# Performance work log

Measured on AMD Instinct MI355X. Metric: run time of the kernel, lower is better.

## Reference

```python
import jax, jax.numpy as jnp
import numpy as np

N, C, H, W = 8, 19, 512, 512


def setup_inputs() -> dict:
    key = jax.random.key(0)
    k1, k2 = jax.random.split(key)
    logits = jax.random.normal(k1, (N, C, H, W), dtype=jnp.float32)
    labels = jax.random.randint(k2, (N, H, W), 0, C, dtype=jnp.int32)
    return {"logits": logits, "labels": labels}


def reference(logits, labels):
    # softmax over class dim, then flatten to [P, C] (P = N*H*W)
    num_classes = logits.shape[1]
    probas = jax.nn.softmax(logits, axis=1)
    probas = jnp.moveaxis(probas, 1, -1).reshape(-1, num_classes)  # [P, C]
    labels_flat = labels.reshape(-1)  # [P]

    # fg[p, c] = 1 if labels[p] == c (ground truth, detached)
    fg = jax.nn.one_hot(labels_flat, num_classes, dtype=probas.dtype)  # [P, C]

    errors = jnp.abs(fg - probas)  # [P, C]
    # per-class descending sort of errors (vectorized over all classes)
    perm = jnp.argsort(-errors, axis=0)  # [P, C]
    errors_sorted = jnp.take_along_axis(errors, perm, axis=0)
    fg_sorted = jnp.take_along_axis(fg, perm, axis=0)

    # Lovasz gradient (Alg. 1), per class column
    gts = jnp.sum(fg_sorted, axis=0)  # [C]
    intersection = gts - jnp.cumsum(fg_sorted, axis=0)  # [P, C]
    union = gts + jnp.cumsum(1.0 - fg_sorted, axis=0)  # [P, C]
    jaccard = 1.0 - intersection / union
    grad = jnp.concatenate([jaccard[:1], jaccard[1:] - jaccard[:-1]], axis=0)

    losses = jnp.sum(errors_sorted * grad, axis=0)  # [C]
    return jnp.mean(losses)
```

## Files before the change

kernel.cpp:

```cpp
#include <hip/hip_runtime.h>

#define CLS   19
#define NBINS 128
#define HWSZ  (512 * 512)
#define NPIX  (8 * HWSZ)
#define HIST  (CLS * NBINS)
#define CSTR  (HIST + 16)
#define NC    2
#define TPB   256
#define NBLK  1024
#define GPB   ((NPIX / 4) / NBLK)

typedef float vf4 __attribute__((ext_vector_type(4)));
typedef int   vi4 __attribute__((ext_vector_type(4)));

__global__ __launch_bounds__(TPB)
void lovasz_zero(unsigned long long* __restrict__ gh, float* __restrict__ out) {
    const int t = threadIdx.x;
    for (int i = t; i < HIST; i += TPB) gh[i] = 0ull;
    if (t == 0) out[0] = 0.f;
}

__global__ __launch_bounds__(TPB)
void lovasz_hist(const float* __restrict__ logits, const int* __restrict__ labels,
                 unsigned long long* __restrict__ gh) {
    __shared__ unsigned h[NC * CSTR];
    const int tid = threadIdx.x;
    for (int i = tid; i < NC * CSTR; i += TPB) h[i] = 0u;
    __syncthreads();

    const unsigned copy = (unsigned)tid & (NC - 1);
    const int base_g = blockIdx.x * GPB;
    for (int it = 0; it < GPB; it += TPB) {
        const int g  = base_g + it + tid;
        const int p  = g << 2;
        const int n  = p >> 18;
        const int hw = p & (HWSZ - 1);
        const vf4* bp = (const vf4*)(logits + (size_t)n * CLS * HWSZ + hw);

        vf4 va[CLS];
#pragma unroll
        for (int c = 0; c < CLS; ++c)
            va[c] = __builtin_nontemporal_load(&bp[c * (HWSZ / 4)]);

        vf4 s = {0.f, 0.f, 0.f, 0.f};
#pragma unroll
        for (int c = 0; c < CLS; ++c) {
            va[c].x = __expf(va[c].x); s.x += va[c].x;
            va[c].y = __expf(va[c].y); s.y += va[c].y;
            va[c].z = __expf(va[c].z); s.z += va[c].z;
            va[c].w = __expf(va[c].w); s.w += va[c].w;
        }
        const vf4 inv = {1.f / s.x, 1.f / s.y, 1.f / s.z, 1.f / s.w};
        const vi4 lab = __builtin_nontemporal_load((const vi4*)(labels + p));

        unsigned* hc = &h[copy * CSTR];
#pragma unroll
        for (int c = 0; c < CLS; ++c) {
            float e; unsigned ic; int b;
            e = va[c].x * inv.x; ic = 1u;
            if (c == lab.x) { e = 1.f - e; ic = 0x10001u; }
            b = (int)(e * (float)NBINS); b = b > (NBINS - 1) ? (NBINS - 1) : b;
            atomicAdd(&hc[c * NBINS + b], ic);
            e = va[c].y * inv.y; ic = 1u;
            if (c == lab.y) { e = 1.f - e; ic = 0x10001u; }
            b = (int)(e * (float)NBINS); b = b > (NBINS - 1) ? (NBINS - 1) : b;
            atomicAdd(&hc[c * NBINS + b], ic);
            e = va[c].z * inv.z; ic = 1u;
            if (c == lab.z) { e = 1.f - e; ic = 0x10001u; }
            b = (int)(e * (float)NBINS); b = b > (NBINS - 1) ? (NBINS - 1) : b;
            atomicAdd(&hc[c * NBINS + b], ic);
            e = va[c].w * inv.w; ic = 1u;
            if (c == lab.w) { e = 1.f - e; ic = 0x10001u; }
            b = (int)(e * (float)NBINS); b = b > (NBINS - 1) ? (NBINS - 1) : b;
            atomicAdd(&hc[c * NBINS + b], ic);
        }
    }
    __syncthreads();
    for (int i = tid; i < HIST; i += TPB) {
        const unsigned v = h[i] + h[CSTR + i];
        if (v) {
            const unsigned long long pk =
                (unsigned long long)(v & 0xFFFFu) | ((unsigned long long)(v >> 16) << 32);
            atomicAdd(&gh[i], pk);
        }
    }
}

__global__ __launch_bounds__(NBINS)
void lovasz_final(const unsigned long long* __restrict__ gh, float* __restrict__ out) {
    __shared__ unsigned scnt[NBINS], sfg[NBINS];
    __shared__ float part[2];
    const int c = blockIdx.x, t = threadIdx.x;

    const unsigned long long v = gh[c * NBINS + t];
    scnt[t] = (unsigned)(v & 0xFFFFFFFFull);
    sfg[t]  = (unsigned)(v >> 32);
    __syncthreads();

    unsigned nb = 0, fb = 0, g = 0;
    for (int b = t + 1; b < NBINS; ++b) { nb += scnt[b]; fb += sfg[b]; }
    for (int b = 0; b < NBINS; ++b) g += sfg[b];

    const float gts = (float)g;
    const float nB = (float)nb,            fB = (float)fb;
    const float nA = nB + (float)scnt[t],  fA = fB + (float)sfg[t];
    const float dB = gts + nB - fB;
    const float jB = dB > 0.f ? 1.f - (gts - fB) / dB : 0.f;
    const float dA = gts + nA - fA;
    const float jA = dA > 0.f ? 1.f - (gts - fA) / dA : 0.f;
    float contrib = (((float)t + 0.5f) * (1.f / NBINS)) * (jA - jB);

    for (int off = 32; off > 0; off >>= 1) contrib += __shfl_down(contrib, off);
    if ((t & 63) == 0) part[t >> 6] = contrib;
    __syncthreads();
    if (t == 0) atomicAdd(out, (part[0] + part[1]) * (1.f / (float)CLS));
}

extern "C" void kernel_launch(void* const* d_in, const int* in_sizes, int n_in,
                              void* d_out, int out_size, void* d_ws, size_t ws_size,
                              hipStream_t stream) {
    const float* logits = (const float*)d_in[0];
    const int*   labels = (const int*)d_in[1];
    float*       out    = (float*)d_out;
    unsigned long long* gh = (unsigned long long*)d_ws;

    lovasz_zero<<<1, TPB, 0, stream>>>(gh, out);
    lovasz_hist<<<NBLK, TPB, 0, stream>>>(logits, labels, gh);
    lovasz_final<<<CLS, NBINS, 0, stream>>>(gh, out);
}
```

Baseline: 234.5 us.

## Fuse final Lovasz reduction into histogram kernel via last-block pattern

Removes the separate final kernel launch: each histogram block increments a global arrival counter, and the last block to arrive computes the per-class Lovasz contributions and writes the output. It also raises the number of shared-memory histogram copies from two to four to reduce atomic contention. The last-block tail runs the 19-class scan serially in one block, and the larger LDS footprint may lower occupancy.

```diff
diff --git a/kernel.cpp b/kernel.cpp
--- a/kernel.cpp
+++ b/kernel.cpp
@@ -5,8 +5,8 @@
 #define HWSZ  (512 * 512)
 #define NPIX  (8 * HWSZ)
 #define HIST  (CLS * NBINS)
-#define CSTR  (HIST + 16)
-#define NC    2
+#define CSTR  (HIST + 8)
+#define NC    4
 #define TPB   256
 #define NBLK  1024
 #define GPB   ((NPIX / 4) / NBLK)
@@ -17,14 +17,16 @@
 __global__ __launch_bounds__(TPB)
 void lovasz_zero(unsigned long long* __restrict__ gh, float* __restrict__ out) {
     const int t = threadIdx.x;
-    for (int i = t; i < HIST; i += TPB) gh[i] = 0ull;
+    for (int i = t; i <= HIST; i += TPB) gh[i] = 0ull;
     if (t == 0) out[0] = 0.f;
 }
 
 __global__ __launch_bounds__(TPB)
 void lovasz_hist(const float* __restrict__ logits, const int* __restrict__ labels,
-                 unsigned long long* __restrict__ gh) {
+                 unsigned long long* __restrict__ gh, float* __restrict__ out) {
     __shared__ unsigned h[NC * CSTR];
+    __shared__ float    part[4];
+    __shared__ unsigned s_arr;
     const int tid = threadIdx.x;
     for (int i = tid; i < NC * CSTR; i += TPB) h[i] = 0u;
     __syncthreads();
@@ -77,44 +79,64 @@
         }
     }
     __syncthreads();
+
     for (int i = tid; i < HIST; i += TPB) {
-        const unsigned v = h[i] + h[CSTR + i];
+        const unsigned v = h[i] + h[CSTR + i] + h[2 * CSTR + i] + h[3 * CSTR + i];
         if (v) {
             const unsigned long long pk =
                 (unsigned long long)(v & 0xFFFFu) | ((unsigned long long)(v >> 16) << 32);
             atomicAdd(&gh[i], pk);
         }
     }
-}
 
-__global__ __launch_bounds__(NBINS)
-void lovasz_final(const unsigned long long* __restrict__ gh, float* __restrict__ out) {
-    __shared__ unsigned scnt[NBINS], sfg[NBINS];
-    __shared__ float part[2];
-    const int c = blockIdx.x, t = threadIdx.x;
+    __threadfence();
+    __syncthreads();
+    if (tid == 0) s_arr = (unsigned)atomicAdd(&gh[HIST], 1ull);
+    __syncthreads();
+    if (s_arr != NBLK - 1) return;
 
-    const unsigned long long v = gh[c * NBINS + t];
-    scnt[t] = (unsigned)(v & 0xFFFFFFFFull);
-    sfg[t]  = (unsigned)(v >> 32);
-    __syncthreads();
+    __threadfence();
+    unsigned* scnt = h;
+    unsigned* sfg  = h + 2 * NBINS;
+    const int bin  = tid & (NBINS - 1);
+    const int half = tid >> 7;
+    float acc = 0.f;
+    for (int cb = 0; cb < CLS; cb += 2) {
+        const int c = cb + half;
+        if (c < CLS) {
+            const unsigned long long v = gh[c * NBINS + bin];
+            scnt[half * NBINS + bin] = (unsigned)(v & 0xFFFFFFFFull);
+            sfg [half * NBINS + bin] = (unsigned)(v >> 32);
+        }
+        __syncthreads();
+        if (c < CLS) {
+            unsigned nb = 0, fb = 0, g = 0;
+            for (int b = bin + 1; b < NBINS; ++b) {
+                nb += scnt[half * NBINS + b]; fb += sfg[half * NBINS + b];
+            }
+            for (int b = 0; b < NBINS; ++b) g += sfg[half * NBINS + b];
 
-    unsigned nb = 0, fb = 0, g = 0;
-    for (int b = t + 1; b < NBINS; ++b) { nb += scnt[b]; fb += sfg[b]; }
-    for (int b = 0; b < NBINS; ++b) g += sfg[b];
+            const float gts = (float)g;
+            const float nB = (float)nb,                           fB = (float)fb;
+            const float nA = nB + (float)scnt[half * NBINS + bin],
+                        fA = fB + (float)sfg [half * NBINS + bin];
+            const float dB = gts + nB - fB;
+            const float jB = dB > 0.f ? 1.f - (gts - fB) / dB : 0.f;
+            const float dA = gts + nA - fA;
+            const float jA = dA > 0.f ? 1.f - (gts - fA) / dA : 0.f;
+            float contrib = (((float)bin + 0.5f) * (1.f / NBINS)) * (jA - jB);
 
-    const float gts = (float)g;
-    const float nB = (float)nb,            fB = (float)fb;
-    const float nA = nB + (float)scnt[t],  fA = fB + (float)sfg[t];
-    const float dB = gts + nB - fB;
-    const float jB = dB > 0.f ? 1.f - (gts - fB) / dB : 0.f;
-    const float dA = gts + nA - fA;
-    const float jA = dA > 0.f ? 1.f - (gts - fA) / dA : 0.f;
-    float contrib = (((float)t + 0.5f) * (1.f / NBINS)) * (jA - jB);
-
-    for (int off = 32; off > 0; off >>= 1) contrib += __shfl_down(contrib, off);
-    if ((t & 63) == 0) part[t >> 6] = contrib;
-    __syncthreads();
-    if (t == 0) atomicAdd(out, (part[0] + part[1]) * (1.f / (float)CLS));
+            for (int off = 32; off > 0; off >>= 1) contrib += __shfl_down(contrib, off);
+            if ((tid & 63) == 0) part[tid >> 6] = contrib;
+        }
+        __syncthreads();
+        if (tid == 0) {
+            acc += (part[0] + part[1]) * (1.f / (float)CLS);
+            if (cb + 1 < CLS) acc += (part[2] + part[3]) * (1.f / (float)CLS);
+        }
+        __syncthreads();
+    }
+    if (tid == 0) out[0] = acc;
 }
 
 extern "C" void kernel_launch(void* const* d_in, const int* in_sizes, int n_in,
@@ -126,6 +148,5 @@
     unsigned long long* gh = (unsigned long long*)d_ws;
 
     lovasz_zero<<<1, TPB, 0, stream>>>(gh, out);
-    lovasz_hist<<<NBLK, TPB, 0, stream>>>(logits, labels, gh);
-    lovasz_final<<<CLS, NBINS, 0, stream>>>(gh, out);
+    lovasz_hist<<<NBLK, TPB, 0, stream>>>(logits, labels, gh, out);
 }
```

Measured after the change: 381.9 us. 62.8% more time.
